# Optimization experiments

Hardware: AMD Instinct MI355X
Metric: run time of the kernel (lower is better)

The kernel has to match this reference:

```python
import jax, jax.numpy as jnp
import numpy as np

HIDDEN = 256
MSG = 256
N_CLASSES = 2


def _ggnn(x, adj, W_lin, b_lin, W_ih, b_ih, W_hh, b_hh, n_timesteps):
    # Append supernode: zero-embedding row to h, ones row + zeros col to adj.
    N = x.shape[0]
    h0 = jnp.concatenate([x, jnp.zeros((1, x.shape[1]), x.dtype)], axis=0)  # [N+1, H]
    A = jnp.concatenate([adj, jnp.ones((1, N), adj.dtype)], axis=0)         # [N+1, N]
    A = jnp.concatenate([A, jnp.zeros((N + 1, 1), adj.dtype)], axis=1)      # [N+1, N+1]

    def step(h, _):
        msgs = h @ W_lin.T + b_lin          # [N+1, MSG] linear projection
        m = A @ msgs                        # [N+1, MSG] message aggregation
        # GRUCell (PyTorch convention): gates order r, z, n
        gi = m @ W_ih.T + b_ih              # [N+1, 3H]
        gh = h @ W_hh.T + b_hh              # [N+1, 3H]
        ir, iz, inn = jnp.split(gi, 3, axis=-1)
        hr, hz, hn = jnp.split(gh, 3, axis=-1)
        r = jax.nn.sigmoid(ir + hr)
        z = jax.nn.sigmoid(iz + hz)
        n = jnp.tanh(inn + r * hn)
        h_new = (1.0 - z) * n + z * h
        return h_new, None

    h, _ = jax.lax.scan(step, h0, None, length=n_timesteps)
    return h


def setup_inputs() -> dict:
    key = jax.random.key(0)
    ks = jax.random.split(key, 12)
    N = 8000
    inp = {
        "b_x": jax.random.normal(ks[0], (N, HIDDEN), dtype=jnp.float32),
        "b_adj": (jax.random.uniform(ks[1], (N, N), dtype=jnp.float32) < 0.002).astype(jnp.float32),
        "a_x": jax.random.normal(ks[2], (N, HIDDEN), dtype=jnp.float32),
        "a_adj": (jax.random.uniform(ks[3], (N, N), dtype=jnp.float32) < 0.002).astype(jnp.float32),
        "W_lin": jax.random.normal(ks[4], (MSG, HIDDEN), dtype=jnp.float32) * 0.05,
        "b_lin": jnp.zeros((MSG,), dtype=jnp.float32),
        "W_ih": jax.random.normal(ks[5], (3 * HIDDEN, MSG), dtype=jnp.float32) * 0.05,
        "b_ih": jnp.zeros((3 * HIDDEN,), dtype=jnp.float32),
        "W_hh": jax.random.normal(ks[6], (3 * HIDDEN, HIDDEN), dtype=jnp.float32) * 0.05,
        "b_hh": jnp.zeros((3 * HIDDEN,), dtype=jnp.float32),
        "W_fc": jax.random.normal(ks[7], (N_CLASSES, 2 * HIDDEN), dtype=jnp.float32) * 0.05,
        "b_fc": jnp.zeros((N_CLASSES,), dtype=jnp.float32),
        "n_timesteps": 8,
    }
    return inp


def reference(b_x, b_adj, a_x, a_adj, W_lin, b_lin, W_ih, b_ih, W_hh, b_hh, W_fc, b_fc, n_timesteps):
    b_h = _ggnn(b_x, b_adj, W_lin, b_lin, W_ih, b_ih, W_hh, b_hh, n_timesteps)
    a_h = _ggnn(a_x, a_adj, W_lin, b_lin, W_ih, b_ih, W_hh, b_hh, n_timesteps)
    supernodes = jnp.concatenate([b_h[-1, :], a_h[-1, :]], axis=0)  # [2H]
    logits = supernodes @ W_fc.T + b_fc                              # [n_classes]
    return jax.nn.log_softmax(logits, axis=0)
```

## Files before the change

kernel.cpp:

```cpp
#include <hip/hip_runtime.h>
#include <hip/hip_bf16.h>
#include <math.h>

#define NNODES 8000
#define NP1    8001
#define H      256
#define CAP    64
#define TSTEPS 8
#define MTOT   (2*NP1)
#define MPAD   16128
#define NRB    (MPAD/32)

typedef __attribute__((ext_vector_type(8))) short short8;
typedef __attribute__((ext_vector_type(4))) float floatx4;

__device__ __forceinline__ float bl2f(unsigned short u) {
  union { unsigned int i; float f; } z; z.i = ((unsigned int)u) << 16; return z.f;
}
__device__ __forceinline__ unsigned short f2bl(float f) {
  __hip_bfloat16 b = __float2bfloat16(f);
  return *(unsigned short*)&b;
}
__device__ __forceinline__ float sigf(float x) { return 1.f / (1.f + __expf(-x)); }
__device__ __forceinline__ float tanhf_fast(float x) { return 2.f / (1.f + __expf(-2.f * x)) - 1.f; }

__global__ __launch_bounds__(256) void build_ell_kernel(
    const float* __restrict__ adj_b, const float* __restrict__ adj_a,
    int* __restrict__ counts, int* __restrict__ colidx)
{
  int w = threadIdx.x >> 6, l = threadIdx.x & 63;
  int b = blockIdx.x * 4 + w;
  int g = b >= NNODES;
  int row = b - g * NNODES;
  const float* adj = (g ? adj_a : adj_b) + (size_t)row * NNODES;
  unsigned long long lt = (1ull << l) - 1;
  int base = 0;
  int* dst = colidx + (size_t)b * CAP;

  #pragma unroll 4
  for (int it = 0; it < 32; ++it) {
    int c0 = it * 256 + l * 4;
    float4 v = (c0 < NNODES) ? *(const float4*)(adj + c0) : make_float4(0, 0, 0, 0);
    bool nz0 = v.x != 0.f, nz1 = v.y != 0.f, nz2 = v.z != 0.f, nz3 = v.w != 0.f;
    bool any = nz0 | nz1 | nz2 | nz3;
    if (__ballot(any)) {
      unsigned long long m0 = __ballot(nz0);
      unsigned long long m1 = __ballot(nz1);
      unsigned long long m2 = __ballot(nz2);
      unsigned long long m3 = __ballot(nz3);
      int t0 = (int)__popcll(m0), t1 = (int)__popcll(m1), t2 = (int)__popcll(m2);
      if (nz0) { int i0 = base + (int)__popcll(m0 & lt);           if (i0 < CAP) dst[i0] = c0; }
      if (nz1) { int i1 = base + t0 + (int)__popcll(m1 & lt);      if (i1 < CAP) dst[i1] = c0 + 1; }
      if (nz2) { int i2 = base + t0 + t1 + (int)__popcll(m2 & lt); if (i2 < CAP) dst[i2] = c0 + 2; }
      if (nz3) { int i3 = base + t0 + t1 + t2 + (int)__popcll(m3 & lt); if (i3 < CAP) dst[i3] = c0 + 3; }
      base += t0 + t1 + t2 + (int)__popcll(m3);
    }
  }
  if (l == 0) counts[b] = base < CAP ? base : CAP;
}

__global__ __launch_bounds__(256) void degf_kernel(
    const int* __restrict__ counts, float* __restrict__ degf)
{
  int row = blockIdx.x * 256 + threadIdx.x;
  float d = 0.f;
  if (row < MTOT) {
    int g = row >= NP1;
    int r = row - g * NP1;
    if (r < NNODES) d = (float)counts[g * NNODES + r];
    else if (r == NNODES) d = (float)NNODES;
  }
  degf[row] = d;
}

__global__ __launch_bounds__(256) void weights_kernel(
    const float* __restrict__ Wih, const float* __restrict__ Wlin,
    const float* __restrict__ blin, const float* __restrict__ Whh,
    __hip_bfloat16* __restrict__ Wbig2, float* __restrict__ bc)
{
  __shared__ float srow[H];
  __shared__ float red[256];
  int p = blockIdx.x;
  int ct32 = p / 96, w96 = p - ct32 * 96;
  int gb = w96 >> 4, u = w96 & 15;
  int jj = gb >> 1, uh = gb & 1;
  int c = ct32 * 32 + uh * 16 + u;
  int gr = jj * 256 + c;
  int t = threadIdx.x;
  size_t ob = (size_t)p * 512;
  srow[t] = Wih[(size_t)gr * H + t];
  __syncthreads();
  float acc = 0.f;
  #pragma unroll 8
  for (int k = 0; k < H; ++k) acc += srow[k] * Wlin[(size_t)k * H + t];
  Wbig2[ob + t] = __float2bfloat16(acc);
  Wbig2[ob + 256 + t] = __float2bfloat16(Whh[(size_t)gr * H + t]);
  red[t] = srow[t] * blin[t];
  __syncthreads();
  for (int s = 128; s > 0; s >>= 1) { if (t < s) red[t] += red[t + s]; __syncthreads(); }
  if (t == 0) bc[gr] = red[0];
}

__global__ __launch_bounds__(256) void init_h_kernel(
    const float* __restrict__ bx, const float* __restrict__ ax,
    __hip_bfloat16* __restrict__ hbf, float* __restrict__ cs0)
{
  int b = blockIdx.x;
  int t = threadIdx.x;
  float l0 = 0.f, l1 = 0.f;
  for (int q = 0; q < 32; ++q) {
    int row = b * 32 + q;
    int g = row >= NP1;
    int r = row - g * NP1;
    float v = 0.f;
    if (r < NNODES) {
      v = (g ? ax : bx)[(size_t)r * H + t];
      if (g) l1 += v; else l0 += v;
    }
    hbf[(size_t)row * H + t] = __float2bfloat16(v);
  }
  if (l0 != 0.f) atomicAdd(&cs0[t], l0);
  if (l1 != 0.f) atomicAdd(&cs0[256 + t], l1);
}

__global__ __launch_bounds__(256) void spmm_kernel(
    const unsigned short* __restrict__ hbf, unsigned short* __restrict__ haggbf,
    const int* __restrict__ counts, const int* __restrict__ colidx,
    const float* __restrict__ cs)
{
  int w = threadIdx.x >> 6, l = threadIdx.x & 63;
  int B = blockIdx.x;
  int g = (B & 7) >= 4;
  int j = (B >> 3) * 4 + (B & 3);
  int r = j * 4 + w;
  if (r > NNODES) return;
  int b = g * NP1 + r;
  size_t outoff = (size_t)b * H + l * 4;
  if (r == NNODES) {
    float4 v = *(const float4*)&cs[g * H + l * 4];
    ushort4 o; o.x = f2bl(v.x); o.y = f2bl(v.y); o.z = f2bl(v.z); o.w = f2bl(v.w);
    *(ushort4*)(haggbf + outoff) = o;
    return;
  }
  int rb = g * NNODES + r;
  int cnt = counts[rb];
  const int* cols = colidx + (size_t)rb * CAP;
  const unsigned short* hg = hbf + (size_t)g * NP1 * H;
  float a0 = 0.f, a1 = 0.f, a2 = 0.f, a3 = 0.f;
  int k = 0;
  for (; k + 4 <= cnt; k += 4) {
    int c0 = cols[k], c1 = cols[k+1], c2 = cols[k+2], c3 = cols[k+3];
    uint2 x0 = *(const uint2*)(hg + (size_t)c0 * H + l * 4);
    uint2 x1 = *(const uint2*)(hg + (size_t)c1 * H + l * 4);
    uint2 x2 = *(const uint2*)(hg + (size_t)c2 * H + l * 4);
    uint2 x3 = *(const uint2*)(hg + (size_t)c3 * H + l * 4);
    a0 += bl2f(x0.x & 0xffff) + bl2f(x1.x & 0xffff) + bl2f(x2.x & 0xffff) + bl2f(x3.x & 0xffff);
    a1 += bl2f(x0.x >> 16)    + bl2f(x1.x >> 16)    + bl2f(x2.x >> 16)    + bl2f(x3.x >> 16);
    a2 += bl2f(x0.y & 0xffff) + bl2f(x1.y & 0xffff) + bl2f(x2.y & 0xffff) + bl2f(x3.y & 0xffff);
    a3 += bl2f(x0.y >> 16)    + bl2f(x1.y >> 16)    + bl2f(x2.y >> 16)    + bl2f(x3.y >> 16);
  }
  for (; k < cnt; ++k) {
    uint2 x = *(const uint2*)(hg + (size_t)cols[k] * H + l * 4);
    a0 += bl2f(x.x & 0xffff); a1 += bl2f(x.x >> 16);
    a2 += bl2f(x.y & 0xffff); a3 += bl2f(x.y >> 16);
  }
  ushort4 o; o.x = f2bl(a0); o.y = f2bl(a1); o.z = f2bl(a2); o.w = f2bl(a3);
  *(ushort4*)(haggbf + outoff) = o;
}

__global__ __launch_bounds__(256, 2) void fused_gemm_gru_kernel(
    const __hip_bfloat16* __restrict__ haggbf, const __hip_bfloat16* __restrict__ hin,
    const __hip_bfloat16* __restrict__ Wbig2, const float* __restrict__ degf,
    const float* __restrict__ bc, const float* __restrict__ bih,
    const float* __restrict__ bhh,
    __hip_bfloat16* __restrict__ hout, float* __restrict__ cs_next)
{
  __shared__ __align__(16) short lsA[256 * 64];
  __shared__ __align__(16) short lsB[96 * 64];
  int bidx = blockIdx.x;
  int ct = bidx >> 6;
  int m_i = bidx & 63;
  if (m_i >= 63) return;
  int m0 = m_i * 256;
  const short* Bbase = (const short*)Wbig2 + (size_t)ct * 96 * 512;
  const short* Ai = (const short*)haggbf;
  const short* Ah = (const short*)hin;
  const unsigned short* hin_us = (const unsigned short*)hin;
  int t = threadIdx.x;
  int w = t >> 6, l = t & 63;
  int lr = l >> 3;
  int lc = l & 7;
  int wm = (w & 1) * 128, uh = w >> 1;
  int q = l >> 4, lm = l & 15;
  floatx4 acc[8][4] = {};

  for (int ks = 0; ks < 8; ++ks) {
    int k0 = ks * 64;
    bool ihalf = ks < 4;
    const short* Asrc = ihalf ? Ai : Ah;
    int ka = k0 & 255;
    #pragma unroll
    for (int j = 0; j < 8; ++j) {
      int r = w * 64 + j * 8 + lr;
      int sc = lc ^ (r & 7);
      const short* ga = Asrc + (size_t)(m0 + r) * H + ka + sc * 8;
      short* la = lsA + (w * 64 + j * 8) * 64;
      __builtin_amdgcn_global_load_lds((const __attribute__((address_space(1))) void*)ga,
                                       (__attribute__((address_space(3))) void*)la, 16, 0, 0);
    }
    #pragma unroll
    for (int j = 0; j < 3; ++j) {
      int r = w * 24 + j * 8 + lr;
      int sc = lc ^ (r & 7);
      const short* gb = Bbase + (size_t)r * 512 + k0 + sc * 8;
      short* lb = lsB + (w * 24 + j * 8) * 64;
      __builtin_amdgcn_global_load_lds((const __attribute__((address_space(1))) void*)gb,
                                       (__attribute__((address_space(3))) void*)lb, 16, 0, 0);
    }
    __syncthreads();
    #pragma unroll
    for (int kh = 0; kh < 2; ++kh) {
      int kc = kh * 4 + q;
      short8 bfr[3];
      #pragma unroll
      for (int jj = 0; jj < 3; ++jj) {
        int n = (jj * 2 + uh) * 16 + lm;
        bfr[jj] = *(const short8*)&lsB[n * 64 + (kc ^ (n & 7)) * 8];
      }
      #pragma unroll
      for (int i = 0; i < 8; ++i) {
        int m = wm + i * 16 + lm;
        short8 af = *(const short8*)&lsA[m * 64 + (kc ^ (m & 7)) * 8];
        acc[i][0] = __builtin_amdgcn_mfma_f32_16x16x32_bf16(af, bfr[0], acc[i][0], 0, 0, 0);
        acc[i][1] = __builtin_amdgcn_mfma_f32_16x16x32_bf16(af, bfr[1], acc[i][1], 0, 0, 0);
        if (ihalf)
          acc[i][2] = __builtin_amdgcn_mfma_f32_16x16x32_bf16(af, bfr[2], acc[i][2], 0, 0, 0);
        else
          acc[i][3] = __builtin_amdgcn_mfma_f32_16x16x32_bf16(af, bfr[2], acc[i][3], 0, 0, 0);
      }
    }
    __syncthreads();
  }

  int c = ct * 32 + uh * 16 + lm;
  float bcr = bc[c], bcz = bc[256 + c], bcn = bc[512 + c];
  float br  = bih[c] + bhh[c];
  float bz  = bih[256 + c] + bhh[256 + c];
  float bin = bih[512 + c];
  float bhn = bhh[512 + c];
  float lu0 = 0.f, lu1 = 0.f;
  #pragma unroll
  for (int i = 0; i < 8; ++i) {
    int row0 = m0 + wm + i * 16 + q * 4;
    float4 dg = *(const float4*)&degf[row0];
    #pragma unroll
    for (int reg = 0; reg < 4; ++reg) {
      int row = row0 + reg;
      float deg = (&dg.x)[reg];
      float rg = sigf(acc[i][0][reg] + deg * bcr + br);
      float z  = sigf(acc[i][1][reg] + deg * bcz + bz);
      float n  = tanhf_fast(acc[i][2][reg] + deg * bcn + bin + rg * (acc[i][3][reg] + bhn));
      size_t hoff = (size_t)row * H + c;
      float hp = bl2f(hin_us[hoff]);
      float hnew = (1.f - z) * n + z * hp;
      hout[hoff] = __float2bfloat16(hnew);
      if (row < NP1) { if (row < NNODES) lu0 += hnew; }
      else { if (row - NP1 < NNODES) lu1 += hnew; }
    }
  }
  lu0 += __shfl_down(lu0, 32); lu0 += __shfl_down(lu0, 16);
  lu1 += __shfl_down(lu1, 32); lu1 += __shfl_down(lu1, 16);
  if (q == 0) {
    if (lu0 != 0.f) atomicAdd(&cs_next[c], lu0);
    if (lu1 != 0.f) atomicAdd(&cs_next[256 + c], lu1);
  }
}

__global__ __launch_bounds__(256) void final_kernel(
    const unsigned short* __restrict__ hbf, const float* __restrict__ Wfc,
    const float* __restrict__ bfc, float* __restrict__ out)
{
  __shared__ float red0[256];
  __shared__ float red1[256];
  int t = threadIdx.x;
  float sn0 = bl2f(hbf[(size_t)NNODES * H + t]);
  float sn1 = bl2f(hbf[((size_t)NP1 + NNODES) * H + t]);
  red0[t] = sn0 * Wfc[t]       + sn1 * Wfc[H + t];
  red1[t] = sn0 * Wfc[512 + t] + sn1 * Wfc[512 + H + t];
  __syncthreads();
  for (int s = 128; s > 0; s >>= 1) {
    if (t < s) { red0[t] += red0[t + s]; red1[t] += red1[t + s]; }
    __syncthreads();
  }
  if (t == 0) {
    float l0 = red0[0] + bfc[0], l1 = red1[0] + bfc[1];
    float m = fmaxf(l0, l1);
    float lse = m + logf(expf(l0 - m) + expf(l1 - m));
    out[0] = l0 - lse;
    out[1] = l1 - lse;
  }
}

extern "C" void kernel_launch(void* const* d_in, const int* in_sizes, int n_in,
                              void* d_out, int out_size, void* d_ws, size_t ws_size,
                              hipStream_t stream) {
  const float* b_x   = (const float*)d_in[0];
  const float* b_adj = (const float*)d_in[1];
  const float* a_x   = (const float*)d_in[2];
  const float* a_adj = (const float*)d_in[3];
  const float* Wlin  = (const float*)d_in[4];
  const float* blin  = (const float*)d_in[5];
  const float* Wih   = (const float*)d_in[6];
  const float* bih   = (const float*)d_in[7];
  const float* Whh   = (const float*)d_in[8];
  const float* bhh   = (const float*)d_in[9];
  const float* Wfc   = (const float*)d_in[10];
  const float* bfc   = (const float*)d_in[11];
  float* out = (float*)d_out;

  char* ws = (char*)d_ws;
  size_t off = 0;
  auto alloc = [&](size_t bytes) {
    void* p = ws + off;
    off += (bytes + 255) & ~(size_t)255;
    return p;
  };
  __hip_bfloat16* hbf0   = (__hip_bfloat16*)alloc((size_t)MPAD * H * 2);
  __hip_bfloat16* hbf1   = (__hip_bfloat16*)alloc((size_t)MPAD * H * 2);
  __hip_bfloat16* haggbf = (__hip_bfloat16*)alloc((size_t)MPAD * H * 2);
  __hip_bfloat16* Wbig2  = (__hip_bfloat16*)alloc((size_t)768 * 512 * 2);
  float* bc              = (float*)alloc((size_t)768 * 4);
  int* colidx            = (int*)alloc((size_t)2 * NNODES * CAP * 4);
  int* counts            = (int*)alloc((size_t)2 * NNODES * 4 + 1024);
  float* degf            = (float*)alloc((size_t)MPAD * 4);
  float* cs              = (float*)alloc((size_t)(TSTEPS + 1) * 2 * H * 4);

  hipMemsetAsync(cs, 0, (size_t)(TSTEPS + 1) * 2 * H * 4, stream);

  build_ell_kernel<<<4000, 256, 0, stream>>>(b_adj, a_adj, counts, colidx);
  degf_kernel<<<MPAD / 256, 256, 0, stream>>>(counts, degf);
  weights_kernel<<<768, 256, 0, stream>>>(Wih, Wlin, blin, Whh, Wbig2, bc);
  init_h_kernel<<<NRB, 256, 0, stream>>>(b_x, a_x, hbf0, cs);

  __hip_bfloat16* ping[2] = { hbf0, hbf1 };
  for (int t = 0; t < TSTEPS; ++t) {
    __hip_bfloat16* hin  = ping[t & 1];
    __hip_bfloat16* hout = ping[(t + 1) & 1];
    spmm_kernel<<<4096, 256, 0, stream>>>(
        (const unsigned short*)hin, (unsigned short*)haggbf, counts, colidx, cs + t * 2 * H);
    fused_gemm_gru_kernel<<<512, 256, 0, stream>>>(
        haggbf, hin, Wbig2, degf, bc, bih, bhh, hout, cs + (t + 1) * 2 * H);
  }
  final_kernel<<<1, 256, 0, stream>>>((const unsigned short*)ping[TSTEPS & 1], Wfc, bfc, out);
}
```

Before: 880.4 us.

## Fuse timestep loop into persistent kernel with software grid barriers

Replaces the per-timestep spmm and fused GEMM/GRU launches with one persistent kernel of 512 blocks. The blocks loop over all timesteps and separate the phases with an atomic-counter grid barrier. The SpMM phase is remapped so each wave handles 8 rows instead of 1, letting the same 512 blocks cover the aggregation. This removes 16 kernel launches and their launch gaps, at the cost of barrier spin overhead, reduced SpMM parallelism, and a deadlock risk if not all blocks are co-resident.

```diff
diff --git a/kernel.cpp b/kernel.cpp
--- a/kernel.cpp
+++ b/kernel.cpp
@@ -10,6 +10,7 @@
 #define MTOT   (2*NP1)
 #define MPAD   16128
 #define NRB    (MPAD/32)
+#define NB     512
 
 typedef __attribute__((ext_vector_type(8))) short short8;
 typedef __attribute__((ext_vector_type(4))) float floatx4;
@@ -23,6 +24,17 @@
 }
 __device__ __forceinline__ float sigf(float x) { return 1.f / (1.f + __expf(-x)); }
 __device__ __forceinline__ float tanhf_fast(float x) { return 2.f / (1.f + __expf(-2.f * x)) - 1.f; }
+
+__device__ __forceinline__ void gbar(int* bar, int target) {
+  __syncthreads();
+  if (threadIdx.x == 0) {
+    __threadfence();
+    atomicAdd(bar, 1);
+    while (atomicAdd(bar, 0) < target) __builtin_amdgcn_s_sleep(16);
+    __threadfence();
+  }
+  __syncthreads();
+}
 
 __global__ __launch_bounds__(256) void build_ell_kernel(
     const float* __restrict__ adj_b, const float* __restrict__ adj_a,
@@ -123,156 +135,163 @@
   if (l1 != 0.f) atomicAdd(&cs0[256 + t], l1);
 }
 
-__global__ __launch_bounds__(256) void spmm_kernel(
-    const unsigned short* __restrict__ hbf, unsigned short* __restrict__ haggbf,
-    const int* __restrict__ counts, const int* __restrict__ colidx,
-    const float* __restrict__ cs)
-{
-  int w = threadIdx.x >> 6, l = threadIdx.x & 63;
-  int B = blockIdx.x;
-  int g = (B & 7) >= 4;
-  int j = (B >> 3) * 4 + (B & 3);
-  int r = j * 4 + w;
-  if (r > NNODES) return;
-  int b = g * NP1 + r;
-  size_t outoff = (size_t)b * H + l * 4;
-  if (r == NNODES) {
-    float4 v = *(const float4*)&cs[g * H + l * 4];
-    ushort4 o; o.x = f2bl(v.x); o.y = f2bl(v.y); o.z = f2bl(v.z); o.w = f2bl(v.w);
-    *(ushort4*)(haggbf + outoff) = o;
-    return;
-  }
-  int rb = g * NNODES + r;
-  int cnt = counts[rb];
-  const int* cols = colidx + (size_t)rb * CAP;
-  const unsigned short* hg = hbf + (size_t)g * NP1 * H;
-  float a0 = 0.f, a1 = 0.f, a2 = 0.f, a3 = 0.f;
-  int k = 0;
-  for (; k + 4 <= cnt; k += 4) {
-    int c0 = cols[k], c1 = cols[k+1], c2 = cols[k+2], c3 = cols[k+3];
-    uint2 x0 = *(const uint2*)(hg + (size_t)c0 * H + l * 4);
-    uint2 x1 = *(const uint2*)(hg + (size_t)c1 * H + l * 4);
-    uint2 x2 = *(const uint2*)(hg + (size_t)c2 * H + l * 4);
-    uint2 x3 = *(const uint2*)(hg + (size_t)c3 * H + l * 4);
-    a0 += bl2f(x0.x & 0xffff) + bl2f(x1.x & 0xffff) + bl2f(x2.x & 0xffff) + bl2f(x3.x & 0xffff);
-    a1 += bl2f(x0.x >> 16)    + bl2f(x1.x >> 16)    + bl2f(x2.x >> 16)    + bl2f(x3.x >> 16);
-    a2 += bl2f(x0.y & 0xffff) + bl2f(x1.y & 0xffff) + bl2f(x2.y & 0xffff) + bl2f(x3.y & 0xffff);
-    a3 += bl2f(x0.y >> 16)    + bl2f(x1.y >> 16)    + bl2f(x2.y >> 16)    + bl2f(x3.y >> 16);
-  }
-  for (; k < cnt; ++k) {
-    uint2 x = *(const uint2*)(hg + (size_t)cols[k] * H + l * 4);
-    a0 += bl2f(x.x & 0xffff); a1 += bl2f(x.x >> 16);
-    a2 += bl2f(x.y & 0xffff); a3 += bl2f(x.y >> 16);
-  }
-  ushort4 o; o.x = f2bl(a0); o.y = f2bl(a1); o.z = f2bl(a2); o.w = f2bl(a3);
-  *(ushort4*)(haggbf + outoff) = o;
-}
-
-__global__ __launch_bounds__(256, 2) void fused_gemm_gru_kernel(
-    const __hip_bfloat16* __restrict__ haggbf, const __hip_bfloat16* __restrict__ hin,
+__global__ __launch_bounds__(256, 2) void loop_kernel(
+    __hip_bfloat16* __restrict__ h0, __hip_bfloat16* __restrict__ h1,
+    __hip_bfloat16* __restrict__ haggbf,
     const __hip_bfloat16* __restrict__ Wbig2, const float* __restrict__ degf,
     const float* __restrict__ bc, const float* __restrict__ bih,
     const float* __restrict__ bhh,
-    __hip_bfloat16* __restrict__ hout, float* __restrict__ cs_next)
+    const int* __restrict__ counts, const int* __restrict__ colidx,
+    float* __restrict__ cs, int* __restrict__ bar)
 {
   __shared__ __align__(16) short lsA[256 * 64];
   __shared__ __align__(16) short lsB[96 * 64];
   int bidx = blockIdx.x;
+  int t = threadIdx.x;
+  int w = t >> 6, l = t & 63;
+  int gA = (bidx & 7) >= 4;
+  int jA = (bidx >> 3) * 4 + (bidx & 3);
   int ct = bidx >> 6;
   int m_i = bidx & 63;
-  if (m_i >= 63) return;
   int m0 = m_i * 256;
   const short* Bbase = (const short*)Wbig2 + (size_t)ct * 96 * 512;
-  const short* Ai = (const short*)haggbf;
-  const short* Ah = (const short*)hin;
-  const unsigned short* hin_us = (const unsigned short*)hin;
-  int t = threadIdx.x;
-  int w = t >> 6, l = t & 63;
-  int lr = l >> 3;
-  int lc = l & 7;
+  int lr = l >> 3, lc = l & 7;
   int wm = (w & 1) * 128, uh = w >> 1;
   int q = l >> 4, lm = l & 15;
-  floatx4 acc[8][4] = {};
-
-  for (int ks = 0; ks < 8; ++ks) {
-    int k0 = ks * 64;
-    bool ihalf = ks < 4;
-    const short* Asrc = ihalf ? Ai : Ah;
-    int ka = k0 & 255;
-    #pragma unroll
-    for (int j = 0; j < 8; ++j) {
-      int r = w * 64 + j * 8 + lr;
-      int sc = lc ^ (r & 7);
-      const short* ga = Asrc + (size_t)(m0 + r) * H + ka + sc * 8;
-      short* la = lsA + (w * 64 + j * 8) * 64;
-      __builtin_amdgcn_global_load_lds((const __attribute__((address_space(1))) void*)ga,
-                                       (__attribute__((address_space(3))) void*)la, 16, 0, 0);
-    }
-    #pragma unroll
-    for (int j = 0; j < 3; ++j) {
-      int r = w * 24 + j * 8 + lr;
-      int sc = lc ^ (r & 7);
-      const short* gb = Bbase + (size_t)r * 512 + k0 + sc * 8;
-      short* lb = lsB + (w * 24 + j * 8) * 64;
-      __builtin_amdgcn_global_load_lds((const __attribute__((address_space(1))) void*)gb,
-                                       (__attribute__((address_space(3))) void*)lb, 16, 0, 0);
-    }
-    __syncthreads();
-    #pragma unroll
-    for (int kh = 0; kh < 2; ++kh) {
-      int kc = kh * 4 + q;
-      short8 bfr[3];
-      #pragma unroll
-      for (int jj = 0; jj < 3; ++jj) {
-        int n = (jj * 2 + uh) * 16 + lm;
-        bfr[jj] = *(const short8*)&lsB[n * 64 + (kc ^ (n & 7)) * 8];
-      }
-      #pragma unroll
-      for (int i = 0; i < 8; ++i) {
-        int m = wm + i * 16 + lm;
-        short8 af = *(const short8*)&lsA[m * 64 + (kc ^ (m & 7)) * 8];
-        acc[i][0] = __builtin_amdgcn_mfma_f32_16x16x32_bf16(af, bfr[0], acc[i][0], 0, 0, 0);
-        acc[i][1] = __builtin_amdgcn_mfma_f32_16x16x32_bf16(af, bfr[1], acc[i][1], 0, 0, 0);
-        if (ihalf)
-          acc[i][2] = __builtin_amdgcn_mfma_f32_16x16x32_bf16(af, bfr[2], acc[i][2], 0, 0, 0);
-        else
-          acc[i][3] = __builtin_amdgcn_mfma_f32_16x16x32_bf16(af, bfr[2], acc[i][3], 0, 0, 0);
-      }
-    }
-    __syncthreads();
-  }
-
   int c = ct * 32 + uh * 16 + lm;
   float bcr = bc[c], bcz = bc[256 + c], bcn = bc[512 + c];
   float br  = bih[c] + bhh[c];
   float bz  = bih[256 + c] + bhh[256 + c];
   float bin = bih[512 + c];
   float bhn = bhh[512 + c];
-  float lu0 = 0.f, lu1 = 0.f;
-  #pragma unroll
-  for (int i = 0; i < 8; ++i) {
-    int row0 = m0 + wm + i * 16 + q * 4;
-    float4 dg = *(const float4*)&degf[row0];
-    #pragma unroll
-    for (int reg = 0; reg < 4; ++reg) {
-      int row = row0 + reg;
-      float deg = (&dg.x)[reg];
-      float rg = sigf(acc[i][0][reg] + deg * bcr + br);
-      float z  = sigf(acc[i][1][reg] + deg * bcz + bz);
-      float n  = tanhf_fast(acc[i][2][reg] + deg * bcn + bin + rg * (acc[i][3][reg] + bhn));
-      size_t hoff = (size_t)row * H + c;
-      float hp = bl2f(hin_us[hoff]);
-      float hnew = (1.f - z) * n + z * hp;
-      hout[hoff] = __float2bfloat16(hnew);
-      if (row < NP1) { if (row < NNODES) lu0 += hnew; }
-      else { if (row - NP1 < NNODES) lu1 += hnew; }
+  int btarget = 0;
+
+  for (int ts = 0; ts < TSTEPS; ++ts) {
+    const unsigned short* hcur = (const unsigned short*)((ts & 1) ? h1 : h0);
+    unsigned short* hnxt = (unsigned short*)((ts & 1) ? h0 : h1);
+    const float* cs_t = cs + ts * 2 * H;
+    float* cs_n = cs + (ts + 1) * 2 * H;
+
+    {
+      unsigned short* hagg_us = (unsigned short*)haggbf;
+      const unsigned short* hg = hcur + (size_t)gA * NP1 * H;
+      #pragma unroll 2
+      for (int e = 0; e < 8; ++e) {
+        int r = (jA * 4 + w) * 8 + e;
+        if (r > NNODES) break;
+        int b = gA * NP1 + r;
+        size_t outoff = (size_t)b * H + l * 4;
+        if (r == NNODES) {
+          float4 v = *(const float4*)&cs_t[gA * H + l * 4];
+          ushort4 o; o.x = f2bl(v.x); o.y = f2bl(v.y); o.z = f2bl(v.z); o.w = f2bl(v.w);
+          *(ushort4*)(hagg_us + outoff) = o;
+          continue;
+        }
+        int rb = gA * NNODES + r;
+        int cnt = counts[rb];
+        const int* cols = colidx + (size_t)rb * CAP;
+        float a0 = 0.f, a1 = 0.f, a2 = 0.f, a3 = 0.f;
+        int k = 0;
+        for (; k + 4 <= cnt; k += 4) {
+          uint2 x0 = *(const uint2*)(hg + (size_t)cols[k]     * H + l * 4);
+          uint2 x1 = *(const uint2*)(hg + (size_t)cols[k + 1] * H + l * 4);
+          uint2 x2 = *(const uint2*)(hg + (size_t)cols[k + 2] * H + l * 4);
+          uint2 x3 = *(const uint2*)(hg + (size_t)cols[k + 3] * H + l * 4);
+          a0 += bl2f(x0.x & 0xffff) + bl2f(x1.x & 0xffff) + bl2f(x2.x & 0xffff) + bl2f(x3.x & 0xffff);
+          a1 += bl2f(x0.x >> 16)    + bl2f(x1.x >> 16)    + bl2f(x2.x >> 16)    + bl2f(x3.x >> 16);
+          a2 += bl2f(x0.y & 0xffff) + bl2f(x1.y & 0xffff) + bl2f(x2.y & 0xffff) + bl2f(x3.y & 0xffff);
+          a3 += bl2f(x0.y >> 16)    + bl2f(x1.y >> 16)    + bl2f(x2.y >> 16)    + bl2f(x3.y >> 16);
+        }
+        for (; k < cnt; ++k) {
+          uint2 x = *(const uint2*)(hg + (size_t)cols[k] * H + l * 4);
+          a0 += bl2f(x.x & 0xffff); a1 += bl2f(x.x >> 16);
+          a2 += bl2f(x.y & 0xffff); a3 += bl2f(x.y >> 16);
+        }
+        ushort4 o; o.x = f2bl(a0); o.y = f2bl(a1); o.z = f2bl(a2); o.w = f2bl(a3);
+        *(ushort4*)(hagg_us + outoff) = o;
+      }
     }
-  }
-  lu0 += __shfl_down(lu0, 32); lu0 += __shfl_down(lu0, 16);
-  lu1 += __shfl_down(lu1, 32); lu1 += __shfl_down(lu1, 16);
-  if (q == 0) {
-    if (lu0 != 0.f) atomicAdd(&cs_next[c], lu0);
-    if (lu1 != 0.f) atomicAdd(&cs_next[256 + c], lu1);
+    btarget += NB; gbar(bar, btarget);
+
+    if (m_i < 63) {
+      const short* Ai = (const short*)haggbf;
+      const short* Ah = (const short*)hcur;
+      floatx4 acc[8][4] = {};
+      for (int ks = 0; ks < 8; ++ks) {
+        int k0 = ks * 64;
+        bool ihalf = ks < 4;
+        const short* Asrc = ihalf ? Ai : Ah;
+        int ka = k0 & 255;
+        #pragma unroll
+        for (int j = 0; j < 8; ++j) {
+          int r = w * 64 + j * 8 + lr;
+          int sc = lc ^ (r & 7);
+          const short* ga = Asrc + (size_t)(m0 + r) * H + ka + sc * 8;
+          short* la = lsA + (w * 64 + j * 8) * 64;
+          __builtin_amdgcn_global_load_lds((const __attribute__((address_space(1))) void*)ga,
+                                           (__attribute__((address_space(3))) void*)la, 16, 0, 0);
+        }
+        #pragma unroll
+        for (int j = 0; j < 3; ++j) {
+          int r = w * 24 + j * 8 + lr;
+          int sc = lc ^ (r & 7);
+          const short* gb = Bbase + (size_t)r * 512 + k0 + sc * 8;
+          short* lb = lsB + (w * 24 + j * 8) * 64;
+          __builtin_amdgcn_global_load_lds((const __attribute__((address_space(1))) void*)gb,
+                                           (__attribute__((address_space(3))) void*)lb, 16, 0, 0);
+        }
+        __syncthreads();
+        #pragma unroll
+        for (int kh = 0; kh < 2; ++kh) {
+          int kc = kh * 4 + q;
+          short8 bfr[3];
+          #pragma unroll
+          for (int jj = 0; jj < 3; ++jj) {
+            int n = (jj * 2 + uh) * 16 + lm;
+            bfr[jj] = *(const short8*)&lsB[n * 64 + (kc ^ (n & 7)) * 8];
+          }
+          #pragma unroll
+          for (int i = 0; i < 8; ++i) {
+            int m = wm + i * 16 + lm;
+            short8 af = *(const short8*)&lsA[m * 64 + (kc ^ (m & 7)) * 8];
+            acc[i][0] = __builtin_amdgcn_mfma_f32_16x16x32_bf16(af, bfr[0], acc[i][0], 0, 0, 0);
+            acc[i][1] = __builtin_amdgcn_mfma_f32_16x16x32_bf16(af, bfr[1], acc[i][1], 0, 0, 0);
+            if (ihalf)
+              acc[i][2] = __builtin_amdgcn_mfma_f32_16x16x32_bf16(af, bfr[2], acc[i][2], 0, 0, 0);
+            else
+              acc[i][3] = __builtin_amdgcn_mfma_f32_16x16x32_bf16(af, bfr[2], acc[i][3], 0, 0, 0);
+          }
+        }
+        __syncthreads();
+      }
+      float lu0 = 0.f, lu1 = 0.f;
+      #pragma unroll
+      for (int i = 0; i < 8; ++i) {
+        int row0 = m0 + wm + i * 16 + q * 4;
+        float4 dg = *(const float4*)&degf[row0];
+        #pragma unroll
+        for (int reg = 0; reg < 4; ++reg) {
+          int row = row0 + reg;
+          float deg = (&dg.x)[reg];
+          float rg = sigf(acc[i][0][reg] + deg * bcr + br);
+          float z  = sigf(acc[i][1][reg] + deg * bcz + bz);
+          float n  = tanhf_fast(acc[i][2][reg] + deg * bcn + bin + rg * (acc[i][3][reg] + bhn));
+          size_t hoff = (size_t)row * H + c;
+          float hp = bl2f(hcur[hoff]);
+          float hnew = (1.f - z) * n + z * hp;
+          hnxt[hoff] = f2bl(hnew);
+          if (row < NP1) { if (row < NNODES) lu0 += hnew; }
+          else { if (row - NP1 < NNODES) lu1 += hnew; }
+        }
+      }
+      lu0 += __shfl_down(lu0, 32); lu0 += __shfl_down(lu0, 16);
+      lu1 += __shfl_down(lu1, 32); lu1 += __shfl_down(lu1, 16);
+      if (q == 0) {
+        if (lu0 != 0.f) atomicAdd(&cs_n[c], lu0);
+        if (lu1 != 0.f) atomicAdd(&cs_n[256 + c], lu1);
+      }
+    }
+    btarget += NB; gbar(bar, btarget);
   }
 }
 
@@ -334,22 +353,18 @@
   int* counts            = (int*)alloc((size_t)2 * NNODES * 4 + 1024);
   float* degf            = (float*)alloc((size_t)MPAD * 4);
   float* cs              = (float*)alloc((size_t)(TSTEPS + 1) * 2 * H * 4);
+  int* bar               = (int*)alloc(256);
 
   hipMemsetAsync(cs, 0, (size_t)(TSTEPS + 1) * 2 * H * 4, stream);
+  hipMemsetAsync(bar, 0, 256, stream);
 
   build_ell_kernel<<<4000, 256, 0, stream>>>(b_adj, a_adj, counts, colidx);
   degf_kernel<<<MPAD / 256, 256, 0, stream>>>(counts, degf);
   weights_kernel<<<768, 256, 0, stream>>>(Wih, Wlin, blin, Whh, Wbig2, bc);
   init_h_kernel<<<NRB, 256, 0, stream>>>(b_x, a_x, hbf0, cs);
 
-  __hip_bfloat16* ping[2] = { hbf0, hbf1 };
-  for (int t = 0; t < TSTEPS; ++t) {
-    __hip_bfloat16* hin  = ping[t & 1];
-    __hip_bfloat16* hout = ping[(t + 1) & 1];
-    spmm_kernel<<<4096, 256, 0, stream>>>(
-        (const unsigned short*)hin, (unsigned short*)haggbf, counts, colidx, cs + t * 2 * H);
-    fused_gemm_gru_kernel<<<512, 256, 0, stream>>>(
-        haggbf, hin, Wbig2, degf, bc, bih, bhh, hout, cs + (t + 1) * 2 * H);
-  }
-  final_kernel<<<1, 256, 0, stream>>>((const unsigned short*)ping[TSTEPS & 1], Wfc, bfc, out);
-}
+  loop_kernel<<<NB, 256, 0, stream>>>(hbf0, hbf1, haggbf, Wbig2, degf,
+                                      bc, bih, bhh, counts, colidx, cs, bar);
+
+  final_kernel<<<1, 256, 0, stream>>>((const unsigned short*)hbf0, Wfc, bfc, out);
+}
```

Result: slower. 2.049 ms (+132.8%).
